# Optimization experiments

Measured on AMD Instinct MI355X. Metric: run time of the kernel, lower is better.

## Reference

```python
import jax, jax.numpy as jnp
import numpy as np

K = 3  # kernel_size

def _hamming2d(k):
    h = np.hamming(k)
    return (np.outer(h, h)).astype(np.float32)

def setup_inputs() -> dict:
    key = jax.random.key(0)
    k1, k2 = jax.random.split(key)
    x = jax.random.normal(k1, (8, 64, 128, 128), dtype=jnp.float32)
    W = jax.random.normal(k2, (9, 64, 3, 3), dtype=jnp.float32) * 0.001
    b = jnp.zeros((9,), dtype=jnp.float32)
    return {"x": x, "W": W, "b": b}

def reference(x, W, b):
    B, C, H, Wd = x.shape
    # filter generator: 3x3 conv, padding=1 -> (B, K*K, H, W)
    mask = jax.lax.conv_general_dilated(
        x, W, window_strides=(1, 1), padding=((1, 1), (1, 1)),
        dimension_numbers=("NCHW", "OIHW", "NCHW")) + b[None, :, None, None]
    # kernel normalizer: softmax over the K*K taps, hamming reweight, renormalize
    mask = jax.nn.softmax(mask, axis=1)
    ham = jnp.asarray(_hamming2d(K).reshape(-1))  # (K*K,)
    mask = mask * ham[None, :, None, None]
    mask = mask / jnp.sum(mask, axis=1, keepdims=True)
    # carafe (up=1): weighted sum of KxK shifted neighborhoods, reflect-padded.
    pad = K // 2
    xp = jnp.pad(x, ((0, 0), (0, 0), (pad, pad), (pad, pad)), mode="reflect")
    lowpass = jnp.zeros_like(x)
    for idx in range(K * K):
        i, j = divmod(idx, K)
        lowpass = lowpass + xp[:, :, i:i + H, j:j + Wd] * mask[:, idx:idx + 1]
    # highpass = x - lowpass; residual output = x + highpass
    return 2.0 * x - lowpass
```

## Files before the change

### kernel.cpp

```cpp
#include <hip/hip_runtime.h>
#include <hip/hip_fp16.h>


typedef __attribute__((ext_vector_type(8))) short short8;
typedef __attribute__((ext_vector_type(4))) float floatx4;
typedef __attribute__((ext_vector_type(4))) unsigned uint4v;

#define IH 128
#define IW 128
#define CCH 64
#define TSX 16
#define TSY 8
#define TPX 18
#define TPY 10
#define CSH 72

__device__ __forceinline__ unsigned cvtpkh(float a, float b) {
    unsigned r;
    asm("v_cvt_pkrtz_f16_f32 %0, %1, %2" : "=v"(r) : "v"(a), "v"(b));
    return r;
}
__device__ __forceinline__ unsigned pkfma_lo(unsigned x2, unsigned m2, unsigned acc) {
    unsigned d;
    asm("v_pk_fma_f16 %0, %1, %2, %3 op_sel:[0,0,0] op_sel_hi:[1,0,1]"
        : "=v"(d) : "v"(x2), "v"(m2), "v"(acc));
    return d;
}
__device__ __forceinline__ unsigned pkfma_hi(unsigned x2, unsigned m2, unsigned acc) {
    unsigned d;
    asm("v_pk_fma_f16 %0, %1, %2, %3 op_sel:[0,1,0] op_sel_hi:[1,1,1]"
        : "=v"(d) : "v"(x2), "v"(m2), "v"(acc));
    return d;
}
__device__ __forceinline__ unsigned pk2xml(unsigned c2, unsigned two2, unsigned l2) {
    unsigned d;
    asm("v_pk_fma_f16 %0, %1, %2, %3 neg_lo:[0,0,1] neg_hi:[0,0,1]"
        : "=v"(d) : "v"(c2), "v"(two2), "v"(l2));
    return d;
}
__device__ __forceinline__ float h2f_lo(unsigned u) {
    return __half2float(__ushort_as_half((unsigned short)(u & 0xFFFFu)));
}
__device__ __forceinline__ float h2f_hi(unsigned u) {
    return __half2float(__ushort_as_half((unsigned short)(u >> 16)));
}
__device__ __forceinline__ unsigned short f2h(float f) {
    return __half_as_ushort(__float2half(f));
}

__global__ __launch_bounds__(128, 2) void ahpf_kernel(
    const float* __restrict__ x, const float* __restrict__ Wg,
    const float* __restrict__ bias, float* __restrict__ out)
{
    __shared__ __align__(16) unsigned short sx[TPY * TPX * CSH];

    const int tid  = threadIdx.x;
    const int lane = tid & 63;
    const int wv   = tid >> 6;

    const unsigned flat = blockIdx.x + 8u * (blockIdx.y + 16u * blockIdx.z);
    const unsigned nid  = (flat & 7u) * 128u + (flat >> 3);
    const int bx = nid & 7, by = (nid >> 3) & 15, bz = nid >> 7;

    const int ty0 = by * TSY;
    const int tx0 = bx * TSX;
    const size_t hw = (size_t)IH * IW;
    const float* xb = x + (size_t)bz * CCH * hw;

    const int fm = lane & 15;
    const int fq = lane >> 4;

    {
        int gx0 = tx0 - 4;
        if (gx0 < 0) gx0 = 0;
        if (gx0 > IW - 24) gx0 = IW - 24;
        const bool xlo = (bx == 0), xhi = (bx == 7);
        const int cg8 = tid & 7;
#pragma unroll
        for (int it = 0; it < 4; ++it) {
            const int s = it * 128 + tid;
            if (s >= 480) break;
            const int u = s >> 3;
            const int y = u / 6, xg = u - 6 * y;
            int gy = ty0 + y - 1;
            gy = gy < 0 ? -gy : (gy >= IH ? 2 * IH - 2 - gy : gy);
            const float* src = xb + (size_t)(cg8 * 8) * hw
                             + (size_t)gy * IW + gx0 + 4 * xg;
            float4 v[8];
#pragma unroll
            for (int jj = 0; jj < 8; ++jj)
                v[jj] = *(const float4*)(src + (size_t)jj * hw);
            const int xbase = gx0 + 4 * xg - tx0 + 1;
#pragma unroll
            for (int e = 0; e < 4; ++e) {
                const float fe[8] = {
                    ((const float*)&v[0])[e], ((const float*)&v[1])[e],
                    ((const float*)&v[2])[e], ((const float*)&v[3])[e],
                    ((const float*)&v[4])[e], ((const float*)&v[5])[e],
                    ((const float*)&v[6])[e], ((const float*)&v[7])[e]};
                uint4v pk;
                pk.x = cvtpkh(fe[0], fe[1]); pk.y = cvtpkh(fe[2], fe[3]);
                pk.z = cvtpkh(fe[4], fe[5]); pk.w = cvtpkh(fe[6], fe[7]);
                const int gxe = gx0 + 4 * xg + e;
                const int xx = xbase + e;
                if (xx >= 0 && xx < TPX)
                    *(uint4v*)&sx[(y * TPX + xx) * CSH + cg8 * 8] = pk;
                if (xlo && gxe == 1)
                    *(uint4v*)&sx[(y * TPX + 0) * CSH + cg8 * 8] = pk;
                if (xhi && gxe == 126)
                    *(uint4v*)&sx[(y * TPX + 17) * CSH + cg8 * 8] = pk;
            }
        }
    }

    short8 afr[18];
#pragma unroll
    for (int s = 0; s < 18; ++s) {
        short8 a = (short8)0;
        if (fm < 9) {
            const int tap = s >> 1, cb = (s & 1) * 32 + fq * 8;
            const float* wp = Wg + fm * 576 + tap;
#pragma unroll
            for (int jj = 0; jj < 8; ++jj)
                a[jj] = (short)f2h(wp[(cb + jj) * 9]);
        }
        afr[s] = a;
    }
    float bq[4];
#pragma unroll
    for (int r = 0; r < 4; ++r) {
        const int t = fq * 4 + r;
        bq[r] = (t < 9) ? bias[t] : 0.0f;
    }

    __syncthreads();

    const bool border = (bx == 0) | (bx == 7) | (by == 0) | (by == 15);
    const int n = fm;

    short8 rbuf[24];
#define FR(dy1, dx1, half) rbuf[(((rr + (dy1)) & 3) * 6) + (dx1) * 2 + (half)]
#define LDSRD(row, dx1, half) \
    (*(const short8*)&sx[((row) * TPX + (n + (dx1))) * CSH + (half) * 32 + fq * 8])

#define CARAFE_TAP(dy1, dx1, qq, HALF)                                       \
    {                                                                        \
        const uint4v A  = *(const uint4v*)&FR(dy1, dx1, 0);                  \
        const uint4v Bv = *(const uint4v*)&FR(dy1, dx1, 1);                  \
        _Pragma("unroll")                                                    \
        for (int u = 0; u < 4; ++u) {                                        \
            l[u]     = pkfma_##HALF(A[u],  qq, l[u]);                        \
            l[4 + u] = pkfma_##HALF(Bv[u], qq, l[4 + u]);                    \
        }                                                                    \
    }

#pragma unroll
    for (int rr = 0; rr < 4; ++rr) {
        const int R = wv * 4 + rr;
        const int h = ty0 + R, w = tx0 + n;

        if (rr == 0) {
#pragma unroll
            for (int dy1 = 0; dy1 < 3; ++dy1)
#pragma unroll
                for (int dx1 = 0; dx1 < 3; ++dx1) {
                    FR(dy1, dx1, 0) = LDSRD(R + dy1, dx1, 0);
                    FR(dy1, dx1, 1) = LDSRD(R + dy1, dx1, 1);
                }
        }

        floatx4 ac0 = {0.f, 0.f, 0.f, 0.f};
        floatx4 ac1 = {0.f, 0.f, 0.f, 0.f};
        if (border) {
#pragma unroll
            for (int dy1 = 0; dy1 < 3; ++dy1)
#pragma unroll
                for (int dx1 = 0; dx1 < 3; ++dx1) {
                    const int hy = h + dy1 - 1, wx = w + dx1 - 1;
                    const bool oob = (hy < 0) | (hy >= IH) | (wx < 0) | (wx >= IW);
                    short8 b0 = FR(dy1, dx1, 0);
                    short8 b1 = FR(dy1, dx1, 1);
                    if (oob) { b0 = (short8)0; b1 = (short8)0; }
                    const int s2 = 2 * (3 * dy1 + dx1);
                    ac0 = __builtin_amdgcn_mfma_f32_16x16x32_f16(afr[s2],     b0, ac0, 0, 0, 0);
                    ac1 = __builtin_amdgcn_mfma_f32_16x16x32_f16(afr[s2 + 1], b1, ac1, 0, 0, 0);
                }
        } else {
#pragma unroll
            for (int dy1 = 0; dy1 < 3; ++dy1)
#pragma unroll
                for (int dx1 = 0; dx1 < 3; ++dx1) {
                    const int s2 = 2 * (3 * dy1 + dx1);
                    ac0 = __builtin_amdgcn_mfma_f32_16x16x32_f16(afr[s2],     FR(dy1, dx1, 0), ac0, 0, 0, 0);
                    ac1 = __builtin_amdgcn_mfma_f32_16x16x32_f16(afr[s2 + 1], FR(dy1, dx1, 1), ac1, 0, 0, 0);
                }
        }
        const floatx4 acc = ac0 + ac1;

        if (rr < 3) {
#pragma unroll
            for (int dx1 = 0; dx1 < 3; ++dx1) {
                rbuf[(((rr + 3) & 3) * 6) + dx1 * 2 + 0] = LDSRD(R + 3, dx1, 0);
                rbuf[(((rr + 3) & 3) * 6) + dx1 * 2 + 1] = LDSRD(R + 3, dx1, 1);
            }
        }

        auto hamt = [](int t) {
            const float a = (t / 3 == 1) ? 1.f : 0.08f;
            const float b = (t % 3 == 1) ? 1.f : 0.08f;
            return a * b;
        };
        const int nval = (fq < 2) ? 4 : (fq == 2 ? 1 : 0);
        float e0 = 0, e1 = 0, e2 = 0, e3 = 0, ssum = 0;
        if (nval >= 1) { e0 = __expf(acc[0] + bq[0]) * hamt(fq * 4 + 0); ssum += e0; }
        if (nval >= 4) { e1 = __expf(acc[1] + bq[1]) * hamt(fq * 4 + 1); ssum += e1;
                         e2 = __expf(acc[2] + bq[2]) * hamt(fq * 4 + 2); ssum += e2;
                         e3 = __expf(acc[3] + bq[3]) * hamt(fq * 4 + 3); ssum += e3; }
        ssum += __shfl_xor(ssum, 16);
        ssum += __shfl_xor(ssum, 32);
        const float inv = 1.0f / ssum;

        const unsigned p01 = cvtpkh(e0 * inv, e1 * inv);
        const unsigned p23 = cvtpkh(e2 * inv, e3 * inv);
        const unsigned q0 = (unsigned)__shfl((int)p01, n);
        const unsigned q1 = (unsigned)__shfl((int)p23, n);
        const unsigned q2 = (unsigned)__shfl((int)p01, 16 + n);
        const unsigned q3 = (unsigned)__shfl((int)p23, 16 + n);
        const unsigned q4 = (unsigned)__shfl((int)p01, 32 + n);

        unsigned l[8];
#pragma unroll
        for (int i = 0; i < 8; ++i) l[i] = 0u;
        CARAFE_TAP(0, 0, q0, lo);
        CARAFE_TAP(0, 1, q0, hi);
        CARAFE_TAP(0, 2, q1, lo);
        CARAFE_TAP(1, 0, q1, hi);
        CARAFE_TAP(1, 1, q2, lo);
        CARAFE_TAP(1, 2, q2, hi);
        CARAFE_TAP(2, 0, q3, lo);
        CARAFE_TAP(2, 1, q3, hi);
        CARAFE_TAP(2, 2, q4, lo);

        const uint4v c0 = *(const uint4v*)&FR(1, 1, 0);
        const uint4v c1 = *(const uint4v*)&FR(1, 1, 1);
        const unsigned TWO2 = 0x40004000u;
        float* ob = out + (size_t)bz * CCH * hw + (size_t)h * IW + w
                  + (size_t)(8 * fq) * hw;
#pragma unroll
        for (int q = 0; q < 4; ++q) {
            const unsigned oe = pk2xml(c0[q], TWO2, l[q]);
            const unsigned oo = pk2xml(c1[q], TWO2, l[4 + q]);
            ob[(size_t)(2 * q) * hw]          = h2f_lo(oe);
            ob[(size_t)(2 * q + 1) * hw]      = h2f_hi(oe);
            ob[(size_t)(32 + 2 * q) * hw]     = h2f_lo(oo);
            ob[(size_t)(32 + 2 * q + 1) * hw] = h2f_hi(oo);
        }
    }
#undef CARAFE_TAP
#undef LDSRD
#undef FR
}

extern "C" void kernel_launch(void* const* d_in, const int* in_sizes, int n_in,
                              void* d_out, int out_size, void* d_ws, size_t ws_size,
                              hipStream_t stream) {
    const float* x    = (const float*)d_in[0];
    const float* Wg   = (const float*)d_in[1];
    const float* bias = (const float*)d_in[2];
    float* out        = (float*)d_out;
    const int B = in_sizes[0] / (CCH * IH * IW);
    dim3 grid(8, 16, B);
    ahpf_kernel<<<grid, dim3(128, 1, 1), 0, stream>>>(x, Wg, bias, out);
}
```

Measured before the change: 111.9 us.

## Prepack fp16 weight fragments in a prep kernel and use 256-thread blocks

```diff
diff --git a/kernel.cpp b/kernel.cpp
--- a/kernel.cpp
+++ b/kernel.cpp
@@ -48,9 +48,28 @@
     return __half_as_ushort(__float2half(f));
 }
 
-__global__ __launch_bounds__(128, 2) void ahpf_kernel(
+__global__ void ahpf_prep(const float* __restrict__ Wg,
+                          unsigned short* __restrict__ wsp)
+{
+    const int i = blockIdx.x * 256 + threadIdx.x;
+    if (i >= 18 * 64) return;
+    const int s = i >> 6, l = i & 63;
+    const int fm = l & 15, fq = l >> 4;
+    const int tap = s >> 1, cb = (s & 1) * 32 + fq * 8;
+    short8 v = (short8)0;
+    if (fm < 9) {
+#pragma unroll
+        for (int jj = 0; jj < 8; ++jj)
+            v[jj] = (short)f2h(Wg[fm * 576 + (cb + jj) * 9 + tap]);
+    }
+    ((short8*)wsp)[i] = v;
+}
+
+template <bool USE_WS>
+__global__ __launch_bounds__(256, 4) void ahpf_kernel(
     const float* __restrict__ x, const float* __restrict__ Wg,
-    const float* __restrict__ bias, float* __restrict__ out)
+    const float* __restrict__ bias, float* __restrict__ out,
+    const unsigned short* __restrict__ wsp)
 {
     __shared__ __align__(16) unsigned short sx[TPY * TPX * CSH];
 
@@ -69,6 +88,32 @@
 
     const int fm = lane & 15;
     const int fq = lane >> 4;
+
+    short8 afr[18];
+    if (USE_WS) {
+        const short8* wf = (const short8*)wsp;
+#pragma unroll
+        for (int s = 0; s < 18; ++s) afr[s] = wf[s * 64 + lane];
+    } else {
+#pragma unroll
+        for (int s = 0; s < 18; ++s) {
+            short8 a = (short8)0;
+            if (fm < 9) {
+                const int tap = s >> 1, cb = (s & 1) * 32 + fq * 8;
+                const float* wp = Wg + fm * 576 + tap;
+#pragma unroll
+                for (int jj = 0; jj < 8; ++jj)
+                    a[jj] = (short)f2h(wp[(cb + jj) * 9]);
+            }
+            afr[s] = a;
+        }
+    }
+    float bq[4];
+#pragma unroll
+    for (int r = 0; r < 4; ++r) {
+        const int t = fq * 4 + r;
+        bq[r] = (t < 9) ? bias[t] : 0.0f;
+    }
 
     {
         int gx0 = tx0 - 4;
@@ -77,8 +122,8 @@
         const bool xlo = (bx == 0), xhi = (bx == 7);
         const int cg8 = tid & 7;
 #pragma unroll
-        for (int it = 0; it < 4; ++it) {
-            const int s = it * 128 + tid;
+        for (int it = 0; it < 2; ++it) {
+            const int s = it * 256 + tid;
             if (s >= 480) break;
             const int u = s >> 3;
             const int y = u / 6, xg = u - 6 * y;
@@ -112,27 +157,6 @@
             }
         }
     }
-
-    short8 afr[18];
-#pragma unroll
-    for (int s = 0; s < 18; ++s) {
-        short8 a = (short8)0;
-        if (fm < 9) {
-            const int tap = s >> 1, cb = (s & 1) * 32 + fq * 8;
-            const float* wp = Wg + fm * 576 + tap;
-#pragma unroll
-            for (int jj = 0; jj < 8; ++jj)
-                a[jj] = (short)f2h(wp[(cb + jj) * 9]);
-        }
-        afr[s] = a;
-    }
-    float bq[4];
-#pragma unroll
-    for (int r = 0; r < 4; ++r) {
-        const int t = fq * 4 + r;
-        bq[r] = (t < 9) ? bias[t] : 0.0f;
-    }
-
     __syncthreads();
 
     const bool border = (bx == 0) | (bx == 7) | (by == 0) | (by == 15);
@@ -155,8 +179,8 @@
     }
 
 #pragma unroll
-    for (int rr = 0; rr < 4; ++rr) {
-        const int R = wv * 4 + rr;
+    for (int rr = 0; rr < 2; ++rr) {
+        const int R = wv * 2 + rr;
         const int h = ty0 + R, w = tx0 + n;
 
         if (rr == 0) {
@@ -197,7 +221,7 @@
         }
         const floatx4 acc = ac0 + ac1;
 
-        if (rr < 3) {
+        if (rr < 1) {
 #pragma unroll
             for (int dx1 = 0; dx1 < 3; ++dx1) {
                 rbuf[(((rr + 3) & 3) * 6) + dx1 * 2 + 0] = LDSRD(R + 3, dx1, 0);
@@ -270,5 +294,12 @@
     float* out        = (float*)d_out;
     const int B = in_sizes[0] / (CCH * IH * IW);
     dim3 grid(8, 16, B);
-    ahpf_kernel<<<grid, dim3(128, 1, 1), 0, stream>>>(x, Wg, bias, out);
-}
+
+    if (ws_size >= 18 * 64 * 16) {
+        unsigned short* wsp = (unsigned short*)d_ws;
+        ahpf_prep<<<5, 256, 0, stream>>>(Wg, wsp);
+        ahpf_kernel<true><<<grid, dim3(256, 1, 1), 0, stream>>>(x, Wg, bias, out, wsp);
+    } else {
+        ahpf_kernel<false><<<grid, dim3(256, 1, 1), 0, stream>>>(x, Wg, bias, out, nullptr);
+    }
+}
```

New measurement: 137.3 us. +22.7%, slower.
